# Performance work log

Hardware: AMD Instinct MI355X
Metric: run time of the kernel (lower is better)

The kernel has to match this reference:

```python
import jax, jax.numpy as jnp
import numpy as np

L_OUT, B, N, C, M, D, T = 4, 4, 1000, 80, 64, 256, 28
CLS_W, L1_W, GIOU_W, MASK_W = 2.0, 5.0, 2.0, 5.0
ALPHA, GAMMA, EPS = 0.25, 2.0, 1e-8
CANDIDATE_K, CENTER_RADIUS, BIG = 10, 2.5, 100000.0


def _areas(b):
    return (b[..., 2] - b[..., 0]) * (b[..., 3] - b[..., 1])


def pairwise_giou(b1, b2):
    # b1 [n,4], b2 [m,4] -> [n,m] generalized IoU (torchvision convention)
    area1, area2 = _areas(b1), _areas(b2)
    lt = jnp.maximum(b1[:, None, :2], b2[None, :, :2])
    rb = jnp.minimum(b1[:, None, 2:], b2[None, :, 2:])
    wh = jnp.clip(rb - lt, 0.0)
    inter = wh[..., 0] * wh[..., 1]
    union = area1[:, None] + area2[None, :] - inter
    iou = inter / union
    lti = jnp.minimum(b1[:, None, :2], b2[None, :, :2])
    rbi = jnp.maximum(b1[:, None, 2:], b2[None, :, 2:])
    whi = jnp.clip(rbi - lti, 0.0)
    areai = whi[..., 0] * whi[..., 1]
    return iou - (areai - union) / areai


def diag_giou(b1, b2):
    # elementwise giou for matched pairs, b1/b2 [n,4] -> [n]
    area1, area2 = _areas(b1), _areas(b2)
    lt = jnp.maximum(b1[:, :2], b2[:, :2])
    rb = jnp.minimum(b1[:, 2:], b2[:, 2:])
    wh = jnp.clip(rb - lt, 0.0)
    inter = wh[:, 0] * wh[:, 1]
    union = area1 + area2 - inter
    iou = inter / union
    lti = jnp.minimum(b1[:, :2], b2[:, :2])
    rbi = jnp.maximum(b1[:, 2:], b2[:, 2:])
    whi = jnp.clip(rbi - lti, 0.0)
    areai = whi[:, 0] * whi[:, 1]
    return iou - (areai - union) / areai


def pairwise_iou(b1, b2, eps=1e-8):
    # mmdet bbox_overlaps, mode='iou'
    area1, area2 = _areas(b1), _areas(b2)
    lt = jnp.maximum(b1[:, None, :2], b2[None, :, :2])
    rb = jnp.minimum(b1[:, None, 2:], b2[None, :, 2:])
    wh = jnp.clip(rb - lt, 0.0)
    inter = wh[..., 0] * wh[..., 1]
    union = jnp.maximum(area1[:, None] + area2[None, :] - inter, eps)
    return inter / union


def simota_match(logits, boxes, gt_cls, gt_boxes, img_size):
    # SimOTA assignment for one image; fixed shapes via masking instead of boolean indexing
    n, c = logits.shape
    m = gt_boxes.shape[0]
    cx = (boxes[:, 0] + boxes[:, 2]) * 0.5
    cy = (boxes[:, 1] + boxes[:, 3]) * 0.5
    w = boxes[:, 2] - boxes[:, 0]
    h = boxes[:, 3] - boxes[:, 1]
    in_gt = ((cx[:, None] > gt_boxes[None, :, 0]) & (cy[:, None] > gt_boxes[None, :, 1])
             & (cx[:, None] < gt_boxes[None, :, 2]) & (cy[:, None] < gt_boxes[None, :, 3]))
    gcx = (gt_boxes[:, 0] + gt_boxes[:, 2]) * 0.5
    gcy = (gt_boxes[:, 1] + gt_boxes[:, 3]) * 0.5
    rx = CENTER_RADIUS * w[:, None]
    ry = CENTER_RADIUS * h[:, None]
    in_ct = ((cx[:, None] > gcx[None, :] - rx) & (cx[:, None] < gcx[None, :] + rx)
             & (cy[:, None] > gcy[None, :] - ry) & (cy[:, None] < gcy[None, :] + ry))
    valid = in_gt.any(1) | in_ct.any(1)
    in_both = in_gt & in_ct
    has_valid = valid.any()
    valid = valid | (~has_valid)          # fallback: all valid when none
    in_both = in_both | (~has_valid)
    # FocalLossCost (mmdet), weight = cls weight
    p = jax.nn.sigmoid(logits)
    neg = -jnp.log(1.0 - p + EPS) * (1.0 - ALPHA) * p ** GAMMA
    pos = -jnp.log(p + EPS) * ALPHA * (1.0 - p) ** GAMMA
    cls_cost = CLS_W * (pos - neg)[:, gt_cls]          # [n,m]
    nb = boxes / img_size
    ngb = gt_boxes / img_size
    l1_cost = L1_W * jnp.abs(nb[:, None, :] - ngb[None, :, :]).sum(-1)
    giou_cost = GIOU_W * (1.0 - pairwise_giou(nb, ngb))
    cost = cls_cost + l1_cost + giou_cost + (~in_both) * BIG
    cost = jnp.where(valid[:, None], cost, 1e15)       # invalid priors never selected
    ious = pairwise_iou(boxes, gt_boxes) * valid[:, None]
    # dynamic_k_matching
    topk_ious, _ = jax.lax.top_k(ious.T, CANDIDATE_K)  # [m,10]
    dyn_k = jnp.maximum(topk_ious.sum(-1).astype(jnp.int32), 1)
    rank = jnp.argsort(jnp.argsort(cost, axis=0), axis=0)
    matching = rank < dyn_k[None, :]                   # [n,m]
    multi = matching.sum(1) > 1
    best = jnp.argmin(cost, axis=1)
    best_oh = best[:, None] == jnp.arange(m)[None, :]
    matching = jnp.where(multi[:, None], best_oh, matching)
    fg = matching.any(1)
    gt_ind = jnp.argmax(matching, axis=1)
    return fg, gt_ind


def per_image_loss(logits, boxes, pfeat, gt_cls, gt_boxes, gt_masks, img_size, w_mask):
    sg = jax.lax.stop_gradient
    fg, gt_ind = simota_match(sg(logits), sg(boxes), gt_cls, sg(gt_boxes), sg(img_size))
    c = logits.shape[1]
    gcls = gt_cls[gt_ind]
    label = jnp.where(fg[:, None], jax.nn.one_hot(gcls, c, dtype=logits.dtype), 0.0)
    # sigmoid focal loss (sum over all n*c logits)
    p = jax.nn.sigmoid(logits)
    ce = -(label * jax.nn.log_sigmoid(logits) + (1.0 - label) * jax.nn.log_sigmoid(-logits))
    p_t = p * label + (1.0 - p) * (1.0 - label)
    alpha_t = ALPHA * label + (1.0 - ALPHA) * (1.0 - label)
    cls_loss = (alpha_t * ce * (1.0 - p_t) ** GAMMA).sum()
    fgf = fg.astype(logits.dtype)
    nb = boxes / img_size
    gb = gt_boxes[gt_ind] / img_size
    l1_loss = (jnp.abs(nb - gb).sum(-1) * fgf).sum()
    giou_loss = ((1.0 - diag_giou(nb, gb)) * fgf).sum()
    # mask head: per-class mask logits from proposal feats; gather only assigned class
    d = pfeat.shape[1]
    tt = T * T
    w_sel = w_mask.reshape(d, c, tt)[:, gcls, :]        # [d,n,tt]
    m_sel = jax.nn.sigmoid(jnp.einsum('nd,dnt->nt', pfeat, w_sel))
    gm = gt_masks.reshape(gt_masks.shape[0], -1)[gt_ind]  # [n,tt]
    inter = (m_sel * gm).sum(-1)
    union = m_sel.sum(-1) + gm.sum(-1) + 1e-8
    mask_loss = ((1.0 - 2.0 * inter / union) * fgf).sum()
    return cls_loss, l1_loss, giou_loss, mask_loss, fgf.sum()


def _forward(pred_logits, pred_boxes, proposal_feat, gt_boxes, gt_masks, image_size, w_mask, gt_classes):
    per = jax.vmap(per_image_loss, in_axes=(0, 0, 0, 0, 0, 0, 0, None))
    total = jnp.zeros(4, dtype=pred_logits.dtype)
    n_out = pred_logits.shape[0]
    for l in range(n_out):   # small fixed loop over output heads
        cl, l1, gl, ml, k = per(pred_logits[l], pred_boxes[l], proposal_feat[l],
                                gt_classes, gt_boxes, gt_masks, image_size, w_mask)
        num_ins = k.sum()
        total = total + jnp.stack([cl.sum(), l1.sum(), gl.sum(), ml.sum()]) / num_ins
    weights = jnp.array([CLS_W, L1_W, GIOU_W, MASK_W], dtype=total.dtype)
    return weights * total / n_out   # [cls, l1, giou, mask] losses


def setup_inputs():
    key = jax.random.key(0)
    ks = jax.random.split(key, 8)

    def rand_boxes(k, shape):
        k1, k2 = jax.random.split(k)
        ctr = jax.random.uniform(k1, shape + (2,), minval=100.0, maxval=700.0)
        wh = jax.random.uniform(k2, shape + (2,), minval=20.0, maxval=300.0)
        return jnp.concatenate([ctr - wh * 0.5, ctr + wh * 0.5], axis=-1)

    pred_logits = jax.random.normal(ks[0], (L_OUT, B, N, C), dtype=jnp.float32)
    pred_boxes = rand_boxes(ks[1], (L_OUT, B, N))
    proposal_feat = 0.1 * jax.random.normal(ks[2], (L_OUT, B, N, D), dtype=jnp.float32)
    gt_boxes = rand_boxes(ks[3], (B, M))
    gt_masks = (jax.random.uniform(ks[4], (B, M, T, T)) > 0.5).astype(jnp.float32)
    image_size = 800.0 * jnp.ones((B,), dtype=jnp.float32)
    w_mask = 0.02 * jax.random.normal(ks[5], (D, C * T * T), dtype=jnp.float32)
    gt_classes = jax.random.randint(ks[6], (B, M), 0, C)
    return {"pred_logits": pred_logits, "pred_boxes": pred_boxes, "proposal_feat": proposal_feat,
            "gt_boxes": gt_boxes, "gt_masks": gt_masks, "image_size": image_size,
            "w_mask": w_mask, "gt_classes": gt_classes}


def reference(pred_logits, pred_boxes, proposal_feat, gt_boxes, gt_masks, image_size, w_mask, gt_classes):
    return _forward(pred_logits, pred_boxes, proposal_feat, gt_boxes, gt_masks, image_size, w_mask, gt_classes)
```

## Files before the change

### kernel.cpp

```cpp
#include <hip/hip_runtime.h>
#include <math.h>
#include <float.h>

#define LOUT 4
#define BATCH 4
#define NP 1000
#define NC 80
#define NM 64
#define ND 256
#define TT 784
#define NIMG (LOUT*BATCH)
#define CWTT (NC*TT)
#define MAXF (NIMG*NP)
#define CH 16
#define TPT 112
#define MAXCH 768

__device__ __forceinline__ float block_reduce_sum(float v, float* red) {
    int tid = threadIdx.x;
    red[tid] = v; __syncthreads();
    for (int s = blockDim.x >> 1; s > 0; s >>= 1) {
        if (tid < s) red[tid] += red[tid + s];
        __syncthreads();
    }
    float r = red[0]; __syncthreads();
    return r;
}

__global__ void __launch_bounds__(256) k_prep(
        const float* __restrict__ logits, const float* __restrict__ boxes,
        const float* __restrict__ gtb, const float* __restrict__ gtm,
        int* __restrict__ valid, unsigned long long* __restrict__ inboth,
        float* __restrict__ logT, float* __restrict__ negsum,
        float* __restrict__ gmsum, float* __restrict__ interA,
        float* __restrict__ msumA, float* __restrict__ accum, int* __restrict__ cnt) {
    int blk = blockIdx.x;
    int tid = threadIdx.x;
    __shared__ float red[256];
    __shared__ float tile[32][33];
    if (blk < 256) {
        int bj = blk;
        float s = 0.f;
        for (int t = tid; t < TT; t += 256) s += gtm[(size_t)bj * TT + t];
        float r = block_reduce_sum(s, red);
        if (tid == 0) gmsum[bj] = r;
    } else if (blk < 320) {
        int rel = blk - 256;
        int img = rel >> 2, q = rel & 3, b = img % BATCH;
        float* g = red;
        g[tid] = gtb[b * NM * 4 + tid];
        __syncthreads();
        int i = q * 256 + tid;
        if (i >= NP) return;
        float4 bx = *(const float4*)&boxes[((size_t)img * NP + i) * 4];
        float x0 = bx.x, y0 = bx.y, x1 = bx.z, y1 = bx.w;
        float cx = (x0 + x1) * 0.5f, cy = (y0 + y1) * 0.5f;
        float w = x1 - x0, h = y1 - y0;
        float rx = 2.5f * w, ry = 2.5f * h;
        bool any_gt = false, any_ct = false;
        unsigned long long ib = 0ull;
        for (int j = 0; j < NM; ++j) {
            float gx0 = g[j*4], gy0 = g[j*4+1], gx1 = g[j*4+2], gy1 = g[j*4+3];
            bool igt = (cx > gx0) && (cy > gy0) && (cx < gx1) && (cy < gy1);
            float gcx = (gx0 + gx1) * 0.5f, gcy = (gy0 + gy1) * 0.5f;
            bool ict = (cx > gcx - rx) && (cx < gcx + rx) && (cy > gcy - ry) && (cy < gcy + ry);
            any_gt |= igt; any_ct |= ict;
            if (igt && ict) ib |= (1ull << j);
        }
        bool v = any_gt || any_ct;
        valid[img * NP + i] = v ? 1 : 0;
        inboth[img * NP + i] = ib;
    } else if (blk < 1856) {
        int rel = blk - 320;
        int img = rel / 96; int r2 = rel % 96;
        int i0 = (r2 / 3) * 32, c0 = (r2 % 3) * 32;
        int tx = tid & 31, ty4 = tid >> 5;
        #pragma unroll
        for (int r = 0; r < 4; ++r) {
            int ty = ty4 + r * 8;
            int i = i0 + ty, c = c0 + tx;
            tile[ty][tx] = (i < NP && c < NC) ? logits[((size_t)img * NP + i) * NC + c] : 0.f;
        }
        __syncthreads();
        #pragma unroll
        for (int r = 0; r < 4; ++r) {
            int ty = ty4 + r * 8;
            int c = c0 + ty, i = i0 + tx;
            if (c < NC && i < NP) logT[((size_t)img * NC + c) * NP + i] = tile[tx][ty];
        }
    } else if (blk < 1920) {
        int rel = blk - 1856;
        int img = rel >> 2, q = rel & 3;
        int i = q * 256 + tid;
        if (i >= NP) return;
        const float* lr = logits + ((size_t)img * NP + i) * NC;
        float s = 0.f;
        #pragma unroll 4
        for (int c = 0; c < NC; ++c) {
            float x = lr[c];
            float p = 1.f / (1.f + expf(-x));
            float ax = fabsf(x);
            float sp = log1pf(expf(-ax));
            float ls_neg = fminf(-x, 0.f) - sp;
            s += 0.75f * (-ls_neg) * p * p;
        }
        negsum[img * NP + i] = s;
    } else if (blk < 2045) {
        int idx = (blk - 1920) * 256 + tid;
        if (idx < 16000) interA[idx] = 0.f;
        else if (idx < 32000) msumA[idx - 16000] = 0.f;
    } else {
        if (tid < 80) accum[tid] = 0.f;
        else if (tid < 160) cnt[tid - 80] = 0;
    }
}

__global__ void __launch_bounds__(256) k_costtopk(
        const float* __restrict__ logT, const float* __restrict__ boxes,
        const float* __restrict__ gtb, const int* __restrict__ gcls_all,
        const float* __restrict__ imsz,
        const int* __restrict__ valid, const unsigned long long* __restrict__ inboth,
        float* __restrict__ cost, float* __restrict__ kthc, int* __restrict__ kthi) {
    int img = blockIdx.y, b = img % BATCH;
    int tid = threadIdx.x;
    int w = tid >> 6, l = tid & 63;
    int j = blockIdx.x * 4 + w;
    float s = imsz[b], inv_s = 1.f / s;
    const float* gj = gtb + (b * NM + j) * 4;
    float gx0 = gj[0], gy0 = gj[1], gx1 = gj[2], gy1 = gj[3];
    int gc = gcls_all[b * NM + j];
    float garea = (gx1 - gx0) * (gy1 - gy0);
    float ngx0 = gx0 * inv_s, ngy0 = gy0 * inv_s, ngx1 = gx1 * inv_s, ngy1 = gy1 * inv_s;
    float ngarea = (ngx1 - ngx0) * (ngy1 - ngy0);
    size_t colbase = ((size_t)img * NM + j) * NP;
    const float* lrow = logT + ((size_t)img * NC + gc) * NP;
    unsigned vmask = 0, ibmask = 0;
    #pragma unroll
    for (int e = 0; e < 16; ++e) {
        int i = e * 64 + l;
        if (i < NP) {
            if (valid[img * NP + i]) vmask |= 1u << e;
            if ((inboth[img * NP + i] >> j) & 1ull) ibmask |= 1u << e;
        }
    }
    int hv = __any(vmask != 0);
    float icv[16], ccv[16];
    #pragma unroll
    for (int e = 0; e < 16; ++e) {
        int i = e * 64 + l;
        if (i < NP) {
            float4 bx = *(const float4*)&boxes[((size_t)img * NP + i) * 4];
            float x0 = bx.x, y0 = bx.y, x1 = bx.z, y1 = bx.w;
            float area = (x1 - x0) * (y1 - y0);
            float ltx = fmaxf(x0, gx0), lty = fmaxf(y0, gy0);
            float rbx = fminf(x1, gx1), rby = fminf(y1, gy1);
            float iw = fmaxf(rbx - ltx, 0.f), ih = fmaxf(rby - lty, 0.f);
            float inter = iw * ih;
            float uni = fmaxf(area + garea - inter, 1e-8f);
            float iou = inter / uni;
            float nx0 = x0 * inv_s, ny0 = y0 * inv_s, nx1 = x1 * inv_s, ny1 = y1 * inv_s;
            float narea = (nx1 - nx0) * (ny1 - ny0);
            float nltx = fmaxf(nx0, ngx0), nlty = fmaxf(ny0, ngy0);
            float nrbx = fminf(nx1, ngx1), nrby = fminf(ny1, ngy1);
            float niw = fmaxf(nrbx - nltx, 0.f), nih = fmaxf(nrby - nlty, 0.f);
            float ninter = niw * nih;
            float nuni = narea + ngarea - ninter;
            float niou = ninter / nuni;
            float ex0 = fminf(nx0, ngx0), ey0 = fminf(ny0, ngy0);
            float ex1 = fmaxf(nx1, ngx1), ey1 = fmaxf(ny1, ngy1);
            float earea = fmaxf(ex1 - ex0, 0.f) * fmaxf(ey1 - ey0, 0.f);
            float giou = niou - (earea - nuni) / earea;
            float giou_cost = 2.f * (1.f - giou);
            float l1 = 5.f * (fabsf(nx0 - ngx0) + fabsf(ny0 - ngy0) + fabsf(nx1 - ngx1) + fabsf(ny1 - ngy1));
            float x = lrow[i];
            float p = 1.f / (1.f + expf(-x));
            float neg = -logf(1.f - p + 1e-8f) * 0.75f * p * p;
            float pos = -logf(p + 1e-8f) * 0.25f * (1.f - p) * (1.f - p);
            float cls = 2.f * (pos - neg);
            bool vld = ((vmask >> e) & 1u) || (hv == 0);
            bool inb = ((ibmask >> e) & 1u) || (hv == 0);
            float cst = cls + l1 + giou_cost + (inb ? 0.f : 100000.f);
            if (!vld) cst = 1e15f;
            cost[colbase + i] = cst;
            ccv[e] = cst;
            icv[e] = vld ? iou : 0.f;
        } else {
            ccv[e] = FLT_MAX;
            icv[e] = -FLT_MAX;
        }
    }
    unsigned cons = 0;
    float ssum = 0.f;
    for (int it = 0; it < 10; ++it) {
        float bv = -FLT_MAX; int bi = 0x7fffffff;
        #pragma unroll
        for (int e = 0; e < 16; ++e) {
            if (cons & (1u << e)) continue;
            float v = icv[e]; int i = e * 64 + l;
            if ((v > bv) || (v == bv && i < bi)) { bv = v; bi = i; }
        }
        #pragma unroll
        for (int sft = 1; sft < 64; sft <<= 1) {
            float ov = __shfl_xor(bv, sft, 64);
            int oi = __shfl_xor(bi, sft, 64);
            if ((ov > bv) || (ov == bv && oi < bi)) { bv = ov; bi = oi; }
        }
        ssum += bv;
        if ((bi & 63) == l) cons |= 1u << (bi >> 6);
    }
    int dk = (int)ssum; if (dk < 1) dk = 1;
    cons = 0;
    float gv = 0.f; int gi = 0;
    for (int it = 0; it < dk; ++it) {
        float bv = FLT_MAX; int bi = 0x7fffffff;
        #pragma unroll
        for (int e = 0; e < 16; ++e) {
            if (cons & (1u << e)) continue;
            float v = ccv[e]; int i = e * 64 + l;
            if ((v < bv) || (v == bv && i < bi)) { bv = v; bi = i; }
        }
        #pragma unroll
        for (int sft = 1; sft < 64; sft <<= 1) {
            float ov = __shfl_xor(bv, sft, 64);
            int oi = __shfl_xor(bi, sft, 64);
            if ((ov < bv) || (ov == bv && oi < bi)) { bv = ov; bi = oi; }
        }
        if ((bi & 63) == l) cons |= 1u << (bi >> 6);
        gv = bv; gi = bi;
    }
    if (l == 0) { kthc[img * NM + j] = gv; kthi[img * NM + j] = gi; }
}

__global__ void k_match(const float* __restrict__ cost,
                        const float* __restrict__ kthc, const int* __restrict__ kthi,
                        const float* __restrict__ boxes, const float* __restrict__ gtb,
                        const float* __restrict__ imsz, const int* __restrict__ gcls_all,
                        const float* __restrict__ negsum, const float* __restrict__ logT,
                        int* __restrict__ fg, int* __restrict__ gt_ind,
                        int* __restrict__ cnt, float* __restrict__ accum) {
    int img = blockIdx.y, b = img % BATCH;
    int i = blockIdx.x * blockDim.x + threadIdx.x;
    __shared__ float skc[NM]; __shared__ int ski[NM];
    __shared__ float red[256];
    if (threadIdx.x < NM) {
        skc[threadIdx.x] = kthc[img * NM + threadIdx.x];
        ski[threadIdx.x] = kthi[img * NM + threadIdx.x];
    }
    __syncthreads();
    float l1 = 0.f, gl = 0.f, f = 0.f, vcls = 0.f;
    if (i < NP) {
        vcls = negsum[img * NP + i];
        int cntm = 0, first = -1;
        float bc = FLT_MAX; int bj = 0;
        for (int j = 0; j < NM; ++j) {
            float c = cost[((size_t)img * NM + j) * NP + i];
            bool m = (c < skc[j]) || (c == skc[j] && i <= ski[j]);
            if (m) { cntm++; if (first < 0) first = j; }
            if (c < bc) { bc = c; bj = j; }
        }
        int gi = 0, isfg = 0;
        if (cntm > 1) { gi = bj; isfg = 1; }
        else if (cntm == 1) { gi = first; isfg = 1; }
        fg[img * NP + i] = isfg;
        gt_ind[img * NP + i] = gi;
        if (isfg) {
            int gc = gcls_all[b * NM + gi];
            atomicAdd(&cnt[gc], 1);
            float x = logT[((size_t)img * NC + gc) * NP + i];
            float p = 1.f / (1.f + expf(-x));
            float ax = fabsf(x);
            float sp = log1pf(expf(-ax));
            float ls_pos = fminf(x, 0.f) - sp;
            float ls_neg = fminf(-x, 0.f) - sp;
            float pos = 0.25f * (-ls_pos) * (1.f - p) * (1.f - p);
            float neg = 0.75f * (-ls_neg) * p * p;
            vcls += pos - neg;
            float inv = 1.f / imsz[b];
            float4 bx = *(const float4*)&boxes[((size_t)img * NP + i) * 4];
            const float* gj = gtb + (b * NM + gi) * 4;
            float nx0 = bx.x*inv, ny0 = bx.y*inv, nx1 = bx.z*inv, ny1 = bx.w*inv;
            float gx0 = gj[0]*inv, gy0 = gj[1]*inv, gx1 = gj[2]*inv, gy1 = gj[3]*inv;
            l1 = fabsf(nx0-gx0) + fabsf(ny0-gy0) + fabsf(nx1-gx1) + fabsf(ny1-gy1);
            float a1 = (nx1-nx0)*(ny1-ny0), a2 = (gx1-gx0)*(gy1-gy0);
            float ltx = fmaxf(nx0,gx0), lty = fmaxf(ny0,gy0);
            float rbx = fminf(nx1,gx1), rby = fminf(ny1,gy1);
            float iw = fmaxf(rbx-ltx,0.f), ih = fmaxf(rby-lty,0.f);
            float inter = iw*ih, uni = a1+a2-inter, iou = inter/uni;
            float ex0 = fminf(nx0,gx0), ey0 = fminf(ny0,gy0);
            float ex1 = fmaxf(nx1,gx1), ey1 = fmaxf(ny1,gy1);
            float ea = fmaxf(ex1-ex0,0.f)*fmaxf(ey1-ey0,0.f);
            float giou = iou - (ea-uni)/ea;
            gl = 1.f - giou;
            f = 1.f;
        }
    }
    float scl = block_reduce_sum(vcls, red);
    float sl1 = block_reduce_sum(l1, red);
    float sgl = block_reduce_sum(gl, red);
    float sf  = block_reduce_sum(f, red);
    if (threadIdx.x == 0) {
        atomicAdd(&accum[img*5+0], scl);
        atomicAdd(&accum[img*5+1], sl1);
        atomicAdd(&accum[img*5+2], sgl);
        atomicAdd(&accum[img*5+4], sf);
    }
}

__global__ void __launch_bounds__(1024) k_scanscatter(
        const int* __restrict__ cnt, const int* __restrict__ fg,
        const int* __restrict__ gti, const int* __restrict__ gcls,
        int* __restrict__ offs_g, int* __restrict__ total,
        int* __restrict__ chtab, int* __restrict__ nch, int* __restrict__ list) {
    __shared__ int offs[NC]; __shared__ int choff[NC]; __shared__ int sfill[NC];
    int tid = threadIdx.x;
    if (tid == 0) {
        int s = 0, m = 0;
        for (int c = 0; c < NC; ++c) {
            offs[c] = s; s += cnt[c];
            choff[c] = m; m += (cnt[c] + CH - 1) / CH;
        }
        *total = s; *nch = m;
    }
    if (tid < NC) sfill[tid] = 0;
    __syncthreads();
    if (tid < NC) {
        offs_g[tid] = offs[tid];
        int n = cnt[tid], co = choff[tid];
        for (int k = 0; k * CH < n; ++k) chtab[co + k] = (tid << 16) | k;
    }
    for (int idx = tid; idx < NIMG * NP; idx += 1024) {
        if (fg[idx]) {
            int img = idx / NP, i = idx % NP, b = img % BATCH;
            int gt = gti[idx];
            int c = gcls[b * NM + gt];
            int pos = offs[c] + atomicAdd(&sfill[c], 1);
            list[pos] = (img << 16) | (gt << 10) | i;
        }
    }
}

__global__ void __launch_bounds__(128) k_mgemm(
        const float* __restrict__ pfeat, const float* __restrict__ wmask,
        const float* __restrict__ gtm, const int* __restrict__ list,
        const int* __restrict__ cnt, const int* __restrict__ offs,
        const int* __restrict__ chtab, const int* __restrict__ nch,
        float* __restrict__ inter, float* __restrict__ msum) {
    int ch = blockIdx.x;
    if (ch >= *nch) return;
    int e = chtab[ch];
    int c = e >> 16, k = e & 0xffff;
    int base = offs[c] + k * CH;
    int P = min(CH, cnt[c] - k * CH);
    int tid = threadIdx.x;
    bool act = (tid < TPT);
    int t = blockIdx.y * TPT + (act ? tid : 0);
    __shared__ float pf[CH][ND];
    __shared__ int sl[CH];
    if (tid < CH) sl[tid] = (tid < P) ? list[base + tid] : 0;
    __syncthreads();
    for (int idx = tid; idx < CH * (ND / 4); idx += 128) {
        int p = idx >> 6, d4 = idx & 63;
        float4 v = {0.f, 0.f, 0.f, 0.f};
        if (p < P) {
            int pk = sl[p];
            int img = pk >> 16, i = pk & 1023;
            v = *(const float4*)&pfeat[((size_t)img * NP + i) * ND + d4 * 4];
        }
        *(float4*)&pf[p][d4 * 4] = v;
    }
    __syncthreads();
    float acc[CH];
    #pragma unroll
    for (int p = 0; p < CH; ++p) acc[p] = 0.f;
    if (act) {
        const float* wr = wmask + (size_t)c * TT + t;
        float4 wq[4];
        #pragma unroll
        for (int q = 0; q < 4; ++q) {
            const float* wp = wr + (size_t)q * 4 * CWTT;
            wq[q].x = wp[0]; wq[q].y = wp[CWTT];
            wq[q].z = wp[2 * (size_t)CWTT]; wq[q].w = wp[3 * (size_t)CWTT];
        }
        #pragma unroll 4
        for (int d4 = 0; d4 < 60; ++d4) {
            float4 w = wq[d4 & 3];
            const float* wp = wr + (size_t)(d4 + 4) * 4 * CWTT;
            wq[d4 & 3].x = wp[0]; wq[d4 & 3].y = wp[CWTT];
            wq[d4 & 3].z = wp[2 * (size_t)CWTT]; wq[d4 & 3].w = wp[3 * (size_t)CWTT];
            int d = d4 * 4;
            #pragma unroll
            for (int p = 0; p < CH; ++p) {
                float4 q4 = *(const float4*)&pf[p][d];
                acc[p] += q4.x * w.x + q4.y * w.y + q4.z * w.z + q4.w * w.w;
            }
        }
        #pragma unroll
        for (int d4 = 60; d4 < 64; ++d4) {
            float4 w = wq[d4 & 3];
            int d = d4 * 4;
            #pragma unroll
            for (int p = 0; p < CH; ++p) {
                float4 q4 = *(const float4*)&pf[p][d];
                acc[p] += q4.x * w.x + q4.y * w.y + q4.z * w.z + q4.w * w.w;
            }
        }
    }
    #pragma unroll 4
    for (int p = 0; p < CH; ++p) {
        if (p >= P) break;
        int pk = sl[p];
        int img = pk >> 16, j = (pk >> 10) & 63, b = img % BATCH;
        float li = 0.f, lm = 0.f;
        if (act) {
            float m = 1.f / (1.f + expf(-acc[p]));
            float g = gtm[((size_t)(b * NM + j)) * TT + t];
            li = m * g; lm = m;
        }
        #pragma unroll
        for (int s = 32; s > 0; s >>= 1) {
            li += __shfl_down(li, s, 64);
            lm += __shfl_down(lm, s, 64);
        }
        if ((tid & 63) == 0) {
            atomicAdd(&inter[base + p], li);
            atomicAdd(&msum[base + p], lm);
        }
    }
}

__global__ void __launch_bounds__(256) k_dicefinal(
        const int* __restrict__ list, const int* __restrict__ total,
        const float* __restrict__ inter, const float* __restrict__ msum,
        const float* __restrict__ gmsum, const float* __restrict__ accum,
        float* __restrict__ out) {
    __shared__ float md[NIMG];
    int tid = threadIdx.x;
    if (tid < NIMG) md[tid] = 0.f;
    __syncthreads();
    int n = *total;
    for (int e = tid; e < n; e += 256) {
        int pk = list[e];
        int img = pk >> 16, j = (pk >> 10) & 63, b = img % BATCH;
        float d = 1.f - 2.f * inter[e] / (msum[e] + gmsum[b * NM + j] + 1e-8f);
        atomicAdd(&md[img], d);
    }
    __syncthreads();
    if (tid == 0) {
        float tot[4] = {0.f, 0.f, 0.f, 0.f};
        for (int l = 0; l < LOUT; ++l) {
            float s0 = 0.f, s1 = 0.f, s2 = 0.f, s3 = 0.f, s4 = 0.f;
            for (int b = 0; b < BATCH; ++b) {
                int img = l * BATCH + b;
                s0 += accum[img*5+0]; s1 += accum[img*5+1]; s2 += accum[img*5+2];
                s3 += md[img];        s4 += accum[img*5+4];
            }
            tot[0] += s0 / s4; tot[1] += s1 / s4; tot[2] += s2 / s4; tot[3] += s3 / s4;
        }
        const float w[4] = {2.f, 5.f, 2.f, 5.f};
        for (int k = 0; k < 4; ++k) out[k] = w[k] * tot[k] / (float)LOUT;
    }
}

extern "C" void kernel_launch(void* const* d_in, const int* in_sizes, int n_in,
                              void* d_out, int out_size, void* d_ws, size_t ws_size,
                              hipStream_t stream) {
    const float* logits = (const float*)d_in[0];
    const float* boxes  = (const float*)d_in[1];
    const float* pfeat  = (const float*)d_in[2];
    const float* gtb    = (const float*)d_in[3];
    const float* gtm    = (const float*)d_in[4];
    const float* imsz   = (const float*)d_in[5];
    const float* wmask  = (const float*)d_in[6];
    const int*   gcls   = (const int*)d_in[7];

    char* ws = (char*)d_ws;
    size_t off = 0;
    auto alloc = [&](size_t bytes) -> void* {
        void* p = ws + off;
        off = (off + bytes + 255) & ~(size_t)255;
        return p;
    };
    float* accum = (float*)alloc(NIMG * 5 * sizeof(float));
    int* cnt    = (int*)alloc(NC * sizeof(int));
    float* interA = (float*)alloc((size_t)MAXF * sizeof(float));
    float* msumA  = (float*)alloc((size_t)MAXF * sizeof(float));
    float* cost = (float*)alloc((size_t)NIMG * NM * NP * sizeof(float));
    float* logT = (float*)alloc((size_t)NIMG * NC * NP * sizeof(float));
    float* negsum = (float*)alloc((size_t)NIMG * NP * sizeof(float));
    int* valid  = (int*)alloc((size_t)NIMG * NP * sizeof(int));
    unsigned long long* inboth = (unsigned long long*)alloc((size_t)NIMG * NP * sizeof(unsigned long long));
    float* kthc = (float*)alloc(NIMG * NM * sizeof(float));
    int* kthi   = (int*)alloc(NIMG * NM * sizeof(int));
    int* fg     = (int*)alloc((size_t)NIMG * NP * sizeof(int));
    int* gti    = (int*)alloc((size_t)NIMG * NP * sizeof(int));
    float* gmsum = (float*)alloc(BATCH * NM * sizeof(float));
    int* offs   = (int*)alloc(NC * sizeof(int));
    int* total  = (int*)alloc(sizeof(int));
    int* nch    = (int*)alloc(sizeof(int));
    int* chtab  = (int*)alloc((size_t)MAXCH * sizeof(int));
    int* list   = (int*)alloc((size_t)MAXF * sizeof(int));

    k_prep<<<2046, 256, 0, stream>>>(logits, boxes, gtb, gtm, valid, inboth,
                                     logT, negsum, gmsum, interA, msumA, accum, cnt);
    k_costtopk<<<dim3(NM / 4, NIMG), 256, 0, stream>>>(logT, boxes, gtb, gcls, imsz, valid, inboth, cost, kthc, kthi);
    k_match<<<dim3((NP + 255) / 256, NIMG), 256, 0, stream>>>(cost, kthc, kthi, boxes, gtb, imsz, gcls, negsum, logT, fg, gti, cnt, accum);
    k_scanscatter<<<1, 1024, 0, stream>>>(cnt, fg, gti, gcls, offs, total, chtab, nch, list);
    k_mgemm<<<dim3(MAXCH, 7), 128, 0, stream>>>(pfeat, wmask, gtm, list, cnt, offs, chtab, nch, interA, msumA);
    k_dicefinal<<<1, 256, 0, stream>>>(list, total, interA, msumA, gmsum, accum, (float*)d_out);
}
```

Baseline: 193.1 us.

## Fuse front stages into cooperative persistent kernel and fold dice final into mgemm

Merges the prep, cost/top-k, match and scan/scatter kernels into one cooperative kernel that uses grid-wide syncs between phases. It also folds the final dice reduction into the mask GEMM kernel through a last-block-done atomic counter. The aim is to cut kernel launch and inter-kernel gaps across six small dependent stages. In exchange it adds grid.sync costs and limits the grid to co-resident blocks, which can reduce parallelism in the phases that have few blocks.

```diff
diff --git a/kernel.cpp b/kernel.cpp
--- a/kernel.cpp
+++ b/kernel.cpp
@@ -1,6 +1,9 @@
 #include <hip/hip_runtime.h>
+#include <hip/hip_cooperative_groups.h>
 #include <math.h>
 #include <float.h>
+
+namespace cg = cooperative_groups;
 
 #define LOUT 4
 #define BATCH 4
@@ -15,6 +18,7 @@
 #define CH 16
 #define TPT 112
 #define MAXCH 768
+#define TOTALB (MAXCH*7)
 
 __device__ __forceinline__ float block_reduce_sum(float v, float* red) {
     int tid = threadIdx.x;
@@ -27,313 +31,309 @@
     return r;
 }
 
-__global__ void __launch_bounds__(256) k_prep(
+__global__ void __launch_bounds__(256) k_front(
         const float* __restrict__ logits, const float* __restrict__ boxes,
         const float* __restrict__ gtb, const float* __restrict__ gtm,
+        const int* __restrict__ gcls, const float* __restrict__ imsz,
         int* __restrict__ valid, unsigned long long* __restrict__ inboth,
         float* __restrict__ logT, float* __restrict__ negsum,
-        float* __restrict__ gmsum, float* __restrict__ interA,
-        float* __restrict__ msumA, float* __restrict__ accum, int* __restrict__ cnt) {
-    int blk = blockIdx.x;
+        float* __restrict__ gmsum, float* __restrict__ interA, float* __restrict__ msumA,
+        float* __restrict__ accum, int* __restrict__ cnt, int* __restrict__ fill,
+        float* __restrict__ cost, float* __restrict__ kthc, int* __restrict__ kthi,
+        int* __restrict__ fg, int* __restrict__ gti,
+        int* __restrict__ offs_g, int* __restrict__ total, int* __restrict__ chtab,
+        int* __restrict__ nch, int* __restrict__ list, int* __restrict__ done, int G) {
+    cg::grid_group grid = cg::this_grid();
     int tid = threadIdx.x;
     __shared__ float red[256];
     __shared__ float tile[32][33];
-    if (blk < 256) {
-        int bj = blk;
-        float s = 0.f;
-        for (int t = tid; t < TT; t += 256) s += gtm[(size_t)bj * TT + t];
-        float r = block_reduce_sum(s, red);
-        if (tid == 0) gmsum[bj] = r;
-    } else if (blk < 320) {
-        int rel = blk - 256;
-        int img = rel >> 2, q = rel & 3, b = img % BATCH;
-        float* g = red;
-        g[tid] = gtb[b * NM * 4 + tid];
-        __syncthreads();
-        int i = q * 256 + tid;
-        if (i >= NP) return;
-        float4 bx = *(const float4*)&boxes[((size_t)img * NP + i) * 4];
-        float x0 = bx.x, y0 = bx.y, x1 = bx.z, y1 = bx.w;
-        float cx = (x0 + x1) * 0.5f, cy = (y0 + y1) * 0.5f;
-        float w = x1 - x0, h = y1 - y0;
-        float rx = 2.5f * w, ry = 2.5f * h;
-        bool any_gt = false, any_ct = false;
-        unsigned long long ib = 0ull;
-        for (int j = 0; j < NM; ++j) {
-            float gx0 = g[j*4], gy0 = g[j*4+1], gx1 = g[j*4+2], gy1 = g[j*4+3];
-            bool igt = (cx > gx0) && (cy > gy0) && (cx < gx1) && (cy < gy1);
-            float gcx = (gx0 + gx1) * 0.5f, gcy = (gy0 + gy1) * 0.5f;
-            bool ict = (cx > gcx - rx) && (cx < gcx + rx) && (cy > gcy - ry) && (cy < gcy + ry);
-            any_gt |= igt; any_ct |= ict;
-            if (igt && ict) ib |= (1ull << j);
-        }
-        bool v = any_gt || any_ct;
-        valid[img * NP + i] = v ? 1 : 0;
-        inboth[img * NP + i] = ib;
-    } else if (blk < 1856) {
-        int rel = blk - 320;
-        int img = rel / 96; int r2 = rel % 96;
-        int i0 = (r2 / 3) * 32, c0 = (r2 % 3) * 32;
-        int tx = tid & 31, ty4 = tid >> 5;
-        #pragma unroll
-        for (int r = 0; r < 4; ++r) {
-            int ty = ty4 + r * 8;
-            int i = i0 + ty, c = c0 + tx;
-            tile[ty][tx] = (i < NP && c < NC) ? logits[((size_t)img * NP + i) * NC + c] : 0.f;
-        }
-        __syncthreads();
-        #pragma unroll
-        for (int r = 0; r < 4; ++r) {
-            int ty = ty4 + r * 8;
-            int c = c0 + ty, i = i0 + tx;
-            if (c < NC && i < NP) logT[((size_t)img * NC + c) * NP + i] = tile[tx][ty];
-        }
-    } else if (blk < 1920) {
-        int rel = blk - 1856;
-        int img = rel >> 2, q = rel & 3;
-        int i = q * 256 + tid;
-        if (i >= NP) return;
-        const float* lr = logits + ((size_t)img * NP + i) * NC;
-        float s = 0.f;
-        #pragma unroll 4
-        for (int c = 0; c < NC; ++c) {
-            float x = lr[c];
-            float p = 1.f / (1.f + expf(-x));
-            float ax = fabsf(x);
-            float sp = log1pf(expf(-ax));
-            float ls_neg = fminf(-x, 0.f) - sp;
-            s += 0.75f * (-ls_neg) * p * p;
-        }
-        negsum[img * NP + i] = s;
-    } else if (blk < 2045) {
-        int idx = (blk - 1920) * 256 + tid;
-        if (idx < 16000) interA[idx] = 0.f;
-        else if (idx < 32000) msumA[idx - 16000] = 0.f;
-    } else {
-        if (tid < 80) accum[tid] = 0.f;
-        else if (tid < 160) cnt[tid - 80] = 0;
-    }
-}
-
-__global__ void __launch_bounds__(256) k_costtopk(
-        const float* __restrict__ logT, const float* __restrict__ boxes,
-        const float* __restrict__ gtb, const int* __restrict__ gcls_all,
-        const float* __restrict__ imsz,
-        const int* __restrict__ valid, const unsigned long long* __restrict__ inboth,
-        float* __restrict__ cost, float* __restrict__ kthc, int* __restrict__ kthi) {
-    int img = blockIdx.y, b = img % BATCH;
-    int tid = threadIdx.x;
-    int w = tid >> 6, l = tid & 63;
-    int j = blockIdx.x * 4 + w;
-    float s = imsz[b], inv_s = 1.f / s;
-    const float* gj = gtb + (b * NM + j) * 4;
-    float gx0 = gj[0], gy0 = gj[1], gx1 = gj[2], gy1 = gj[3];
-    int gc = gcls_all[b * NM + j];
-    float garea = (gx1 - gx0) * (gy1 - gy0);
-    float ngx0 = gx0 * inv_s, ngy0 = gy0 * inv_s, ngx1 = gx1 * inv_s, ngy1 = gy1 * inv_s;
-    float ngarea = (ngx1 - ngx0) * (ngy1 - ngy0);
-    size_t colbase = ((size_t)img * NM + j) * NP;
-    const float* lrow = logT + ((size_t)img * NC + gc) * NP;
-    unsigned vmask = 0, ibmask = 0;
-    #pragma unroll
-    for (int e = 0; e < 16; ++e) {
-        int i = e * 64 + l;
-        if (i < NP) {
-            if (valid[img * NP + i]) vmask |= 1u << e;
-            if ((inboth[img * NP + i] >> j) & 1ull) ibmask |= 1u << e;
-        }
-    }
-    int hv = __any(vmask != 0);
-    float icv[16], ccv[16];
-    #pragma unroll
-    for (int e = 0; e < 16; ++e) {
-        int i = e * 64 + l;
-        if (i < NP) {
-            float4 bx = *(const float4*)&boxes[((size_t)img * NP + i) * 4];
-            float x0 = bx.x, y0 = bx.y, x1 = bx.z, y1 = bx.w;
-            float area = (x1 - x0) * (y1 - y0);
-            float ltx = fmaxf(x0, gx0), lty = fmaxf(y0, gy0);
-            float rbx = fminf(x1, gx1), rby = fminf(y1, gy1);
-            float iw = fmaxf(rbx - ltx, 0.f), ih = fmaxf(rby - lty, 0.f);
-            float inter = iw * ih;
-            float uni = fmaxf(area + garea - inter, 1e-8f);
-            float iou = inter / uni;
-            float nx0 = x0 * inv_s, ny0 = y0 * inv_s, nx1 = x1 * inv_s, ny1 = y1 * inv_s;
-            float narea = (nx1 - nx0) * (ny1 - ny0);
-            float nltx = fmaxf(nx0, ngx0), nlty = fmaxf(ny0, ngy0);
-            float nrbx = fminf(nx1, ngx1), nrby = fminf(ny1, ngy1);
-            float niw = fmaxf(nrbx - nltx, 0.f), nih = fmaxf(nrby - nlty, 0.f);
-            float ninter = niw * nih;
-            float nuni = narea + ngarea - ninter;
-            float niou = ninter / nuni;
-            float ex0 = fminf(nx0, ngx0), ey0 = fminf(ny0, ngy0);
-            float ex1 = fmaxf(nx1, ngx1), ey1 = fmaxf(ny1, ngy1);
-            float earea = fmaxf(ex1 - ex0, 0.f) * fmaxf(ey1 - ey0, 0.f);
-            float giou = niou - (earea - nuni) / earea;
-            float giou_cost = 2.f * (1.f - giou);
-            float l1 = 5.f * (fabsf(nx0 - ngx0) + fabsf(ny0 - ngy0) + fabsf(nx1 - ngx1) + fabsf(ny1 - ngy1));
-            float x = lrow[i];
-            float p = 1.f / (1.f + expf(-x));
-            float neg = -logf(1.f - p + 1e-8f) * 0.75f * p * p;
-            float pos = -logf(p + 1e-8f) * 0.25f * (1.f - p) * (1.f - p);
-            float cls = 2.f * (pos - neg);
-            bool vld = ((vmask >> e) & 1u) || (hv == 0);
-            bool inb = ((ibmask >> e) & 1u) || (hv == 0);
-            float cst = cls + l1 + giou_cost + (inb ? 0.f : 100000.f);
-            if (!vld) cst = 1e15f;
-            cost[colbase + i] = cst;
-            ccv[e] = cst;
-            icv[e] = vld ? iou : 0.f;
+    __shared__ float skc[NM]; __shared__ int ski[NM];
+    __shared__ int loffs[NC]; __shared__ int lchoff[NC];
+
+    for (int vb = blockIdx.x; vb < 2046; vb += G) {
+        if (vb < 256) {
+            int bj = vb;
+            float s = 0.f;
+            for (int t = tid; t < TT; t += 256) s += gtm[(size_t)bj * TT + t];
+            float r = block_reduce_sum(s, red);
+            if (tid == 0) gmsum[bj] = r;
+        } else if (vb < 320) {
+            int rel = vb - 256;
+            int img = rel >> 2, q = rel & 3, b = img % BATCH;
+            red[tid] = gtb[b * NM * 4 + tid];
+            __syncthreads();
+            int i = q * 256 + tid;
+            if (i < NP) {
+                float4 bx = *(const float4*)&boxes[((size_t)img * NP + i) * 4];
+                float x0 = bx.x, y0 = bx.y, x1 = bx.z, y1 = bx.w;
+                float cx = (x0 + x1) * 0.5f, cy = (y0 + y1) * 0.5f;
+                float w = x1 - x0, h = y1 - y0;
+                float rx = 2.5f * w, ry = 2.5f * h;
+                bool any_gt = false, any_ct = false;
+                unsigned long long ib = 0ull;
+                for (int j = 0; j < NM; ++j) {
+                    float gx0 = red[j*4], gy0 = red[j*4+1], gx1 = red[j*4+2], gy1 = red[j*4+3];
+                    bool igt = (cx > gx0) && (cy > gy0) && (cx < gx1) && (cy < gy1);
+                    float gcx = (gx0 + gx1) * 0.5f, gcy = (gy0 + gy1) * 0.5f;
+                    bool ict = (cx > gcx - rx) && (cx < gcx + rx) && (cy > gcy - ry) && (cy < gcy + ry);
+                    any_gt |= igt; any_ct |= ict;
+                    if (igt && ict) ib |= (1ull << j);
+                }
+                valid[img * NP + i] = (any_gt || any_ct) ? 1 : 0;
+                inboth[img * NP + i] = ib;
+            }
+        } else if (vb < 1856) {
+            int rel = vb - 320;
+            int img = rel / 96; int r2 = rel % 96;
+            int i0 = (r2 / 3) * 32, c0 = (r2 % 3) * 32;
+            int tx = tid & 31, ty4 = tid >> 5;
+            #pragma unroll
+            for (int r = 0; r < 4; ++r) {
+                int ty = ty4 + r * 8;
+                int i = i0 + ty, c = c0 + tx;
+                tile[ty][tx] = (i < NP && c < NC) ? logits[((size_t)img * NP + i) * NC + c] : 0.f;
+            }
+            __syncthreads();
+            #pragma unroll
+            for (int r = 0; r < 4; ++r) {
+                int ty = ty4 + r * 8;
+                int c = c0 + ty, i = i0 + tx;
+                if (c < NC && i < NP) logT[((size_t)img * NC + c) * NP + i] = tile[tx][ty];
+            }
+        } else if (vb < 1920) {
+            int rel = vb - 1856;
+            int img = rel >> 2, q = rel & 3;
+            int i = q * 256 + tid;
+            if (i < NP) {
+                const float* lr = logits + ((size_t)img * NP + i) * NC;
+                float s = 0.f;
+                #pragma unroll 4
+                for (int c = 0; c < NC; ++c) {
+                    float x = lr[c];
+                    float p = 1.f / (1.f + expf(-x));
+                    float ax = fabsf(x);
+                    float sp = log1pf(expf(-ax));
+                    float ls_neg = fminf(-x, 0.f) - sp;
+                    s += 0.75f * (-ls_neg) * p * p;
+                }
+                negsum[img * NP + i] = s;
+            }
+        } else if (vb < 2045) {
+            int idx = (vb - 1920) * 256 + tid;
+            if (idx < 16000) interA[idx] = 0.f;
+            else if (idx < 32000) msumA[idx - 16000] = 0.f;
         } else {
-            ccv[e] = FLT_MAX;
-            icv[e] = -FLT_MAX;
-        }
-    }
-    unsigned cons = 0;
-    float ssum = 0.f;
-    for (int it = 0; it < 10; ++it) {
-        float bv = -FLT_MAX; int bi = 0x7fffffff;
+            if (tid < 80) accum[tid] = 0.f;
+            else if (tid < 160) cnt[tid - 80] = 0;
+            else if (tid < 240) fill[tid - 160] = 0;
+            else if (tid == 240) *done = 0;
+        }
+        __syncthreads();
+    }
+    grid.sync();
+
+    for (int vb = blockIdx.x; vb < 256; vb += G) {
+        int img = vb >> 4, b = img % BATCH;
+        int w = tid >> 6, l = tid & 63;
+        int j = ((vb & 15) << 2) + w;
+        float s = imsz[b], inv_s = 1.f / s;
+        const float* gj = gtb + (b * NM + j) * 4;
+        float gx0 = gj[0], gy0 = gj[1], gx1 = gj[2], gy1 = gj[3];
+        int gc = gcls[b * NM + j];
+        float garea = (gx1 - gx0) * (gy1 - gy0);
+        float ngx0 = gx0 * inv_s, ngy0 = gy0 * inv_s, ngx1 = gx1 * inv_s, ngy1 = gy1 * inv_s;
+        float ngarea = (ngx1 - ngx0) * (ngy1 - ngy0);
+        size_t colbase = ((size_t)img * NM + j) * NP;
+        const float* lrow = logT + ((size_t)img * NC + gc) * NP;
+        unsigned vmask = 0, ibmask = 0;
         #pragma unroll
         for (int e = 0; e < 16; ++e) {
-            if (cons & (1u << e)) continue;
-            float v = icv[e]; int i = e * 64 + l;
-            if ((v > bv) || (v == bv && i < bi)) { bv = v; bi = i; }
-        }
-        #pragma unroll
-        for (int sft = 1; sft < 64; sft <<= 1) {
-            float ov = __shfl_xor(bv, sft, 64);
-            int oi = __shfl_xor(bi, sft, 64);
-            if ((ov > bv) || (ov == bv && oi < bi)) { bv = ov; bi = oi; }
-        }
-        ssum += bv;
-        if ((bi & 63) == l) cons |= 1u << (bi >> 6);
-    }
-    int dk = (int)ssum; if (dk < 1) dk = 1;
-    cons = 0;
-    float gv = 0.f; int gi = 0;
-    for (int it = 0; it < dk; ++it) {
-        float bv = FLT_MAX; int bi = 0x7fffffff;
+            int i = e * 64 + l;
+            if (i < NP) {
+                if (valid[img * NP + i]) vmask |= 1u << e;
+                if ((inboth[img * NP + i] >> j) & 1ull) ibmask |= 1u << e;
+            }
+        }
+        int hv = __any(vmask != 0);
+        float icv[16], ccv[16];
         #pragma unroll
         for (int e = 0; e < 16; ++e) {
-            if (cons & (1u << e)) continue;
-            float v = ccv[e]; int i = e * 64 + l;
-            if ((v < bv) || (v == bv && i < bi)) { bv = v; bi = i; }
-        }
-        #pragma unroll
-        for (int sft = 1; sft < 64; sft <<= 1) {
-            float ov = __shfl_xor(bv, sft, 64);
-            int oi = __shfl_xor(bi, sft, 64);
-            if ((ov < bv) || (ov == bv && oi < bi)) { bv = ov; bi = oi; }
-        }
-        if ((bi & 63) == l) cons |= 1u << (bi >> 6);
-        gv = bv; gi = bi;
-    }
-    if (l == 0) { kthc[img * NM + j] = gv; kthi[img * NM + j] = gi; }
-}
-
-__global__ void k_match(const float* __restrict__ cost,
-                        const float* __restrict__ kthc, const int* __restrict__ kthi,
-                        const float* __restrict__ boxes, const float* __restrict__ gtb,
-                        const float* __restrict__ imsz, const int* __restrict__ gcls_all,
-                        const float* __restrict__ negsum, const float* __restrict__ logT,
-                        int* __restrict__ fg, int* __restrict__ gt_ind,
-                        int* __restrict__ cnt, float* __restrict__ accum) {
-    int img = blockIdx.y, b = img % BATCH;
-    int i = blockIdx.x * blockDim.x + threadIdx.x;
-    __shared__ float skc[NM]; __shared__ int ski[NM];
-    __shared__ float red[256];
-    if (threadIdx.x < NM) {
-        skc[threadIdx.x] = kthc[img * NM + threadIdx.x];
-        ski[threadIdx.x] = kthi[img * NM + threadIdx.x];
-    }
-    __syncthreads();
-    float l1 = 0.f, gl = 0.f, f = 0.f, vcls = 0.f;
-    if (i < NP) {
-        vcls = negsum[img * NP + i];
-        int cntm = 0, first = -1;
-        float bc = FLT_MAX; int bj = 0;
-        for (int j = 0; j < NM; ++j) {
-            float c = cost[((size_t)img * NM + j) * NP + i];
-            bool m = (c < skc[j]) || (c == skc[j] && i <= ski[j]);
-            if (m) { cntm++; if (first < 0) first = j; }
-            if (c < bc) { bc = c; bj = j; }
-        }
-        int gi = 0, isfg = 0;
-        if (cntm > 1) { gi = bj; isfg = 1; }
-        else if (cntm == 1) { gi = first; isfg = 1; }
-        fg[img * NP + i] = isfg;
-        gt_ind[img * NP + i] = gi;
-        if (isfg) {
-            int gc = gcls_all[b * NM + gi];
-            atomicAdd(&cnt[gc], 1);
-            float x = logT[((size_t)img * NC + gc) * NP + i];
-            float p = 1.f / (1.f + expf(-x));
-            float ax = fabsf(x);
-            float sp = log1pf(expf(-ax));
-            float ls_pos = fminf(x, 0.f) - sp;
-            float ls_neg = fminf(-x, 0.f) - sp;
-            float pos = 0.25f * (-ls_pos) * (1.f - p) * (1.f - p);
-            float neg = 0.75f * (-ls_neg) * p * p;
-            vcls += pos - neg;
-            float inv = 1.f / imsz[b];
-            float4 bx = *(const float4*)&boxes[((size_t)img * NP + i) * 4];
-            const float* gj = gtb + (b * NM + gi) * 4;
-            float nx0 = bx.x*inv, ny0 = bx.y*inv, nx1 = bx.z*inv, ny1 = bx.w*inv;
-            float gx0 = gj[0]*inv, gy0 = gj[1]*inv, gx1 = gj[2]*inv, gy1 = gj[3]*inv;
-            l1 = fabsf(nx0-gx0) + fabsf(ny0-gy0) + fabsf(nx1-gx1) + fabsf(ny1-gy1);
-            float a1 = (nx1-nx0)*(ny1-ny0), a2 = (gx1-gx0)*(gy1-gy0);
-            float ltx = fmaxf(nx0,gx0), lty = fmaxf(ny0,gy0);
-            float rbx = fminf(nx1,gx1), rby = fminf(ny1,gy1);
-            float iw = fmaxf(rbx-ltx,0.f), ih = fmaxf(rby-lty,0.f);
-            float inter = iw*ih, uni = a1+a2-inter, iou = inter/uni;
-            float ex0 = fminf(nx0,gx0), ey0 = fminf(ny0,gy0);
-            float ex1 = fmaxf(nx1,gx1), ey1 = fmaxf(ny1,gy1);
-            float ea = fmaxf(ex1-ex0,0.f)*fmaxf(ey1-ey0,0.f);
-            float giou = iou - (ea-uni)/ea;
-            gl = 1.f - giou;
-            f = 1.f;
-        }
-    }
-    float scl = block_reduce_sum(vcls, red);
-    float sl1 = block_reduce_sum(l1, red);
-    float sgl = block_reduce_sum(gl, red);
-    float sf  = block_reduce_sum(f, red);
-    if (threadIdx.x == 0) {
-        atomicAdd(&accum[img*5+0], scl);
-        atomicAdd(&accum[img*5+1], sl1);
-        atomicAdd(&accum[img*5+2], sgl);
-        atomicAdd(&accum[img*5+4], sf);
-    }
-}
-
-__global__ void __launch_bounds__(1024) k_scanscatter(
-        const int* __restrict__ cnt, const int* __restrict__ fg,
-        const int* __restrict__ gti, const int* __restrict__ gcls,
-        int* __restrict__ offs_g, int* __restrict__ total,
-        int* __restrict__ chtab, int* __restrict__ nch, int* __restrict__ list) {
-    __shared__ int offs[NC]; __shared__ int choff[NC]; __shared__ int sfill[NC];
-    int tid = threadIdx.x;
+            int i = e * 64 + l;
+            if (i < NP) {
+                float4 bx = *(const float4*)&boxes[((size_t)img * NP + i) * 4];
+                float x0 = bx.x, y0 = bx.y, x1 = bx.z, y1 = bx.w;
+                float area = (x1 - x0) * (y1 - y0);
+                float ltx = fmaxf(x0, gx0), lty = fmaxf(y0, gy0);
+                float rbx = fminf(x1, gx1), rby = fminf(y1, gy1);
+                float iw = fmaxf(rbx - ltx, 0.f), ih = fmaxf(rby - lty, 0.f);
+                float inter = iw * ih;
+                float uni = fmaxf(area + garea - inter, 1e-8f);
+                float iou = inter / uni;
+                float nx0 = x0 * inv_s, ny0 = y0 * inv_s, nx1 = x1 * inv_s, ny1 = y1 * inv_s;
+                float narea = (nx1 - nx0) * (ny1 - ny0);
+                float nltx = fmaxf(nx0, ngx0), nlty = fmaxf(ny0, ngy0);
+                float nrbx = fminf(nx1, ngx1), nrby = fminf(ny1, ngy1);
+                float niw = fmaxf(nrbx - nltx, 0.f), nih = fmaxf(nrby - nlty, 0.f);
+                float ninter = niw * nih;
+                float nuni = narea + ngarea - ninter;
+                float niou = ninter / nuni;
+                float ex0 = fminf(nx0, ngx0), ey0 = fminf(ny0, ngy0);
+                float ex1 = fmaxf(nx1, ngx1), ey1 = fmaxf(ny1, ngy1);
+                float earea = fmaxf(ex1 - ex0, 0.f) * fmaxf(ey1 - ey0, 0.f);
+                float giou = niou - (earea - nuni) / earea;
+                float giou_cost = 2.f * (1.f - giou);
+                float l1 = 5.f * (fabsf(nx0 - ngx0) + fabsf(ny0 - ngy0) + fabsf(nx1 - ngx1) + fabsf(ny1 - ngy1));
+                float x = lrow[i];
+                float p = 1.f / (1.f + expf(-x));
+                float neg = -logf(1.f - p + 1e-8f) * 0.75f * p * p;
+                float pos = -logf(p + 1e-8f) * 0.25f * (1.f - p) * (1.f - p);
+                float cls = 2.f * (pos - neg);
+                bool vld = ((vmask >> e) & 1u) || (hv == 0);
+                bool inb = ((ibmask >> e) & 1u) || (hv == 0);
+                float cst = cls + l1 + giou_cost + (inb ? 0.f : 100000.f);
+                if (!vld) cst = 1e15f;
+                cost[colbase + i] = cst;
+                ccv[e] = cst;
+                icv[e] = vld ? iou : 0.f;
+            } else {
+                ccv[e] = FLT_MAX;
+                icv[e] = -FLT_MAX;
+            }
+        }
+        unsigned cons = 0;
+        float ssum = 0.f;
+        for (int it = 0; it < 10; ++it) {
+            float bv = -FLT_MAX; int bi = 0x7fffffff;
+            #pragma unroll
+            for (int e = 0; e < 16; ++e) {
+                if (cons & (1u << e)) continue;
+                float v = icv[e]; int i = e * 64 + l;
+                if ((v > bv) || (v == bv && i < bi)) { bv = v; bi = i; }
+            }
+            #pragma unroll
+            for (int sft = 1; sft < 64; sft <<= 1) {
+                float ov = __shfl_xor(bv, sft, 64);
+                int oi = __shfl_xor(bi, sft, 64);
+                if ((ov > bv) || (ov == bv && oi < bi)) { bv = ov; bi = oi; }
+            }
+            ssum += bv;
+            if ((bi & 63) == l) cons |= 1u << (bi >> 6);
+        }
+        int dk = (int)ssum; if (dk < 1) dk = 1;
+        cons = 0;
+        float gv = 0.f; int gi = 0;
+        for (int it = 0; it < dk; ++it) {
+            float bv = FLT_MAX; int bi = 0x7fffffff;
+            #pragma unroll
+            for (int e = 0; e < 16; ++e) {
+                if (cons & (1u << e)) continue;
+                float v = ccv[e]; int i = e * 64 + l;
+                if ((v < bv) || (v == bv && i < bi)) { bv = v; bi = i; }
+            }
+            #pragma unroll
+            for (int sft = 1; sft < 64; sft <<= 1) {
+                float ov = __shfl_xor(bv, sft, 64);
+                int oi = __shfl_xor(bi, sft, 64);
+                if ((ov < bv) || (ov == bv && oi < bi)) { bv = ov; bi = oi; }
+            }
+            if ((bi & 63) == l) cons |= 1u << (bi >> 6);
+            gv = bv; gi = bi;
+        }
+        if (l == 0) { kthc[img * NM + j] = gv; kthi[img * NM + j] = gi; }
+    }
+    grid.sync();
+
+    for (int vb = blockIdx.x; vb < 64; vb += G) {
+        int img = vb >> 2, b = img % BATCH;
+        int i = ((vb & 3) << 8) + tid;
+        if (tid < NM) {
+            skc[tid] = kthc[img * NM + tid];
+            ski[tid] = kthi[img * NM + tid];
+        }
+        __syncthreads();
+        float l1 = 0.f, gl = 0.f, f = 0.f, vcls = 0.f;
+        if (i < NP) {
+            vcls = negsum[img * NP + i];
+            int cntm = 0, first = -1;
+            float bc = FLT_MAX; int bj = 0;
+            for (int j = 0; j < NM; ++j) {
+                float c = cost[((size_t)img * NM + j) * NP + i];
+                bool m = (c < skc[j]) || (c == skc[j] && i <= ski[j]);
+                if (m) { cntm++; if (first < 0) first = j; }
+                if (c < bc) { bc = c; bj = j; }
+            }
+            int gi = 0, isfg = 0;
+            if (cntm > 1) { gi = bj; isfg = 1; }
+            else if (cntm == 1) { gi = first; isfg = 1; }
+            fg[img * NP + i] = isfg;
+            gti[img * NP + i] = gi;
+            if (isfg) {
+                int gc = gcls[b * NM + gi];
+                atomicAdd(&cnt[gc], 1);
+                float x = logT[((size_t)img * NC + gc) * NP + i];
+                float p = 1.f / (1.f + expf(-x));
+                float ax = fabsf(x);
+                float sp = log1pf(expf(-ax));
+                float ls_pos = fminf(x, 0.f) - sp;
+                float ls_neg = fminf(-x, 0.f) - sp;
+                float pos = 0.25f * (-ls_pos) * (1.f - p) * (1.f - p);
+                float neg = 0.75f * (-ls_neg) * p * p;
+                vcls += pos - neg;
+                float inv = 1.f / imsz[b];
+                float4 bx = *(const float4*)&boxes[((size_t)img * NP + i) * 4];
+                const float* gj = gtb + (b * NM + gi) * 4;
+                float nx0 = bx.x*inv, ny0 = bx.y*inv, nx1 = bx.z*inv, ny1 = bx.w*inv;
+                float gx0 = gj[0]*inv, gy0 = gj[1]*inv, gx1 = gj[2]*inv, gy1 = gj[3]*inv;
+                l1 = fabsf(nx0-gx0) + fabsf(ny0-gy0) + fabsf(nx1-gx1) + fabsf(ny1-gy1);
+                float a1 = (nx1-nx0)*(ny1-ny0), a2 = (gx1-gx0)*(gy1-gy0);
+                float ltx = fmaxf(nx0,gx0), lty = fmaxf(ny0,gy0);
+                float rbx = fminf(nx1,gx1), rby = fminf(ny1,gy1);
+                float iw = fmaxf(rbx-ltx,0.f), ih = fmaxf(rby-lty,0.f);
+                float inter = iw*ih, uni = a1+a2-inter, iou = inter/uni;
+                float ex0 = fminf(nx0,gx0), ey0 = fminf(ny0,gy0);
+                float ex1 = fmaxf(nx1,gx1), ey1 = fmaxf(ny1,gy1);
+                float ea = fmaxf(ex1-ex0,0.f)*fmaxf(ey1-ey0,0.f);
+                float giou = iou - (ea-uni)/ea;
+                gl = 1.f - giou;
+                f = 1.f;
+            }
+        }
+        float scl = block_reduce_sum(vcls, red);
+        float sl1 = block_reduce_sum(l1, red);
+        float sgl = block_reduce_sum(gl, red);
+        float sf  = block_reduce_sum(f, red);
+        if (tid == 0) {
+            atomicAdd(&accum[img*5+0], scl);
+            atomicAdd(&accum[img*5+1], sl1);
+            atomicAdd(&accum[img*5+2], sgl);
+            atomicAdd(&accum[img*5+4], sf);
+        }
+        __syncthreads();
+    }
+    grid.sync();
+
     if (tid == 0) {
         int s = 0, m = 0;
         for (int c = 0; c < NC; ++c) {
-            offs[c] = s; s += cnt[c];
-            choff[c] = m; m += (cnt[c] + CH - 1) / CH;
-        }
-        *total = s; *nch = m;
-    }
-    if (tid < NC) sfill[tid] = 0;
+            loffs[c] = s; s += cnt[c];
+            lchoff[c] = m; m += (cnt[c] + CH - 1) / CH;
+        }
+        if (blockIdx.x == 0) { *total = s; *nch = m; }
+    }
     __syncthreads();
-    if (tid < NC) {
-        offs_g[tid] = offs[tid];
-        int n = cnt[tid], co = choff[tid];
-        for (int k = 0; k * CH < n; ++k) chtab[co + k] = (tid << 16) | k;
-    }
-    for (int idx = tid; idx < NIMG * NP; idx += 1024) {
+    if (blockIdx.x == 0) {
+        if (tid < NC) {
+            offs_g[tid] = loffs[tid];
+            int n = cnt[tid], co = lchoff[tid];
+            for (int k = 0; k * CH < n; ++k) chtab[co + k] = (tid << 16) | k;
+        }
+    }
+    for (int idx = blockIdx.x * 256 + tid; idx < NIMG * NP; idx += G * 256) {
         if (fg[idx]) {
             int img = idx / NP, i = idx % NP, b = img % BATCH;
             int gt = gti[idx];
             int c = gcls[b * NM + gt];
-            int pos = offs[c] + atomicAdd(&sfill[c], 1);
+            int pos = loffs[c] + atomicAdd(&fill[c], 1);
             list[pos] = (img << 16) | (gt << 10) | i;
         }
     }
@@ -344,120 +344,127 @@
         const float* __restrict__ gtm, const int* __restrict__ list,
         const int* __restrict__ cnt, const int* __restrict__ offs,
         const int* __restrict__ chtab, const int* __restrict__ nch,
-        float* __restrict__ inter, float* __restrict__ msum) {
+        float* __restrict__ inter, float* __restrict__ msum,
+        const float* __restrict__ gmsum, const int* __restrict__ total,
+        const float* __restrict__ accum, int* __restrict__ done,
+        float* __restrict__ out) {
     int ch = blockIdx.x;
-    if (ch >= *nch) return;
-    int e = chtab[ch];
-    int c = e >> 16, k = e & 0xffff;
-    int base = offs[c] + k * CH;
-    int P = min(CH, cnt[c] - k * CH);
     int tid = threadIdx.x;
-    bool act = (tid < TPT);
-    int t = blockIdx.y * TPT + (act ? tid : 0);
     __shared__ float pf[CH][ND];
     __shared__ int sl[CH];
-    if (tid < CH) sl[tid] = (tid < P) ? list[base + tid] : 0;
+    __shared__ int lastf;
+    __shared__ float md[NIMG];
+    bool active = (ch < *nch);
+    if (active) {
+        int e = chtab[ch];
+        int c = e >> 16, k = e & 0xffff;
+        int base = offs[c] + k * CH;
+        int P = min(CH, cnt[c] - k * CH);
+        bool act = (tid < TPT);
+        int t = blockIdx.y * TPT + (act ? tid : 0);
+        if (tid < CH) sl[tid] = (tid < P) ? list[base + tid] : 0;
+        __syncthreads();
+        for (int idx = tid; idx < CH * (ND / 4); idx += 128) {
+            int p = idx >> 6, d4 = idx & 63;
+            float4 v = {0.f, 0.f, 0.f, 0.f};
+            if (p < P) {
+                int pk = sl[p];
+                int img = pk >> 16, i = pk & 1023;
+                v = *(const float4*)&pfeat[((size_t)img * NP + i) * ND + d4 * 4];
+            }
+            *(float4*)&pf[p][d4 * 4] = v;
+        }
+        __syncthreads();
+        float acc[CH];
+        #pragma unroll
+        for (int p = 0; p < CH; ++p) acc[p] = 0.f;
+        if (act) {
+            const float* wr = wmask + (size_t)c * TT + t;
+            float4 wq[4];
+            #pragma unroll
+            for (int q = 0; q < 4; ++q) {
+                const float* wp = wr + (size_t)q * 4 * CWTT;
+                wq[q].x = wp[0]; wq[q].y = wp[CWTT];
+                wq[q].z = wp[2 * (size_t)CWTT]; wq[q].w = wp[3 * (size_t)CWTT];
+            }
+            #pragma unroll 4
+            for (int d4 = 0; d4 < 60; ++d4) {
+                float4 w = wq[d4 & 3];
+                const float* wp = wr + (size_t)(d4 + 4) * 4 * CWTT;
+                wq[d4 & 3].x = wp[0]; wq[d4 & 3].y = wp[CWTT];
+                wq[d4 & 3].z = wp[2 * (size_t)CWTT]; wq[d4 & 3].w = wp[3 * (size_t)CWTT];
+                int d = d4 * 4;
+                #pragma unroll
+                for (int p = 0; p < CH; ++p) {
+                    float4 q4 = *(const float4*)&pf[p][d];
+                    acc[p] += q4.x * w.x + q4.y * w.y + q4.z * w.z + q4.w * w.w;
+                }
+            }
+            #pragma unroll
+            for (int d4 = 60; d4 < 64; ++d4) {
+                float4 w = wq[d4 & 3];
+                int d = d4 * 4;
+                #pragma unroll
+                for (int p = 0; p < CH; ++p) {
+                    float4 q4 = *(const float4*)&pf[p][d];
+                    acc[p] += q4.x * w.x + q4.y * w.y + q4.z * w.z + q4.w * w.w;
+                }
+            }
+        }
+        int P2 = P;
+        #pragma unroll 4
+        for (int p = 0; p < CH; ++p) {
+            if (p >= P2) break;
+            int pk = sl[p];
+            int img = pk >> 16, j = (pk >> 10) & 63, b = img % BATCH;
+            float li = 0.f, lm = 0.f;
+            if (act) {
+                float m = 1.f / (1.f + expf(-acc[p]));
+                float g = gtm[((size_t)(b * NM + j)) * TT + t];
+                li = m * g; lm = m;
+            }
+            #pragma unroll
+            for (int s = 32; s > 0; s >>= 1) {
+                li += __shfl_down(li, s, 64);
+                lm += __shfl_down(lm, s, 64);
+            }
+            if ((tid & 63) == 0) {
+                atomicAdd(&inter[base + p], li);
+                atomicAdd(&msum[base + p], lm);
+            }
+        }
+    }
+    __threadfence();
+    if (tid == 0) lastf = (atomicAdd(done, 1) == TOTALB - 1);
     __syncthreads();
-    for (int idx = tid; idx < CH * (ND / 4); idx += 128) {
-        int p = idx >> 6, d4 = idx & 63;
-        float4 v = {0.f, 0.f, 0.f, 0.f};
-        if (p < P) {
-            int pk = sl[p];
-            int img = pk >> 16, i = pk & 1023;
-            v = *(const float4*)&pfeat[((size_t)img * NP + i) * ND + d4 * 4];
-        }
-        *(float4*)&pf[p][d4 * 4] = v;
-    }
-    __syncthreads();
-    float acc[CH];
-    #pragma unroll
-    for (int p = 0; p < CH; ++p) acc[p] = 0.f;
-    if (act) {
-        const float* wr = wmask + (size_t)c * TT + t;
-        float4 wq[4];
-        #pragma unroll
-        for (int q = 0; q < 4; ++q) {
-            const float* wp = wr + (size_t)q * 4 * CWTT;
-            wq[q].x = wp[0]; wq[q].y = wp[CWTT];
-            wq[q].z = wp[2 * (size_t)CWTT]; wq[q].w = wp[3 * (size_t)CWTT];
-        }
-        #pragma unroll 4
-        for (int d4 = 0; d4 < 60; ++d4) {
-            float4 w = wq[d4 & 3];
-            const float* wp = wr + (size_t)(d4 + 4) * 4 * CWTT;
-            wq[d4 & 3].x = wp[0]; wq[d4 & 3].y = wp[CWTT];
-            wq[d4 & 3].z = wp[2 * (size_t)CWTT]; wq[d4 & 3].w = wp[3 * (size_t)CWTT];
-            int d = d4 * 4;
-            #pragma unroll
-            for (int p = 0; p < CH; ++p) {
-                float4 q4 = *(const float4*)&pf[p][d];
-                acc[p] += q4.x * w.x + q4.y * w.y + q4.z * w.z + q4.w * w.w;
-            }
-        }
-        #pragma unroll
-        for (int d4 = 60; d4 < 64; ++d4) {
-            float4 w = wq[d4 & 3];
-            int d = d4 * 4;
-            #pragma unroll
-            for (int p = 0; p < CH; ++p) {
-                float4 q4 = *(const float4*)&pf[p][d];
-                acc[p] += q4.x * w.x + q4.y * w.y + q4.z * w.z + q4.w * w.w;
-            }
-        }
-    }
-    #pragma unroll 4
-    for (int p = 0; p < CH; ++p) {
-        if (p >= P) break;
-        int pk = sl[p];
-        int img = pk >> 16, j = (pk >> 10) & 63, b = img % BATCH;
-        float li = 0.f, lm = 0.f;
-        if (act) {
-            float m = 1.f / (1.f + expf(-acc[p]));
-            float g = gtm[((size_t)(b * NM + j)) * TT + t];
-            li = m * g; lm = m;
-        }
-        #pragma unroll
-        for (int s = 32; s > 0; s >>= 1) {
-            li += __shfl_down(li, s, 64);
-            lm += __shfl_down(lm, s, 64);
-        }
-        if ((tid & 63) == 0) {
-            atomicAdd(&inter[base + p], li);
-            atomicAdd(&msum[base + p], lm);
-        }
-    }
-}
-
-__global__ void __launch_bounds__(256) k_dicefinal(
-        const int* __restrict__ list, const int* __restrict__ total,
-        const float* __restrict__ inter, const float* __restrict__ msum,
-        const float* __restrict__ gmsum, const float* __restrict__ accum,
-        float* __restrict__ out) {
-    __shared__ float md[NIMG];
-    int tid = threadIdx.x;
-    if (tid < NIMG) md[tid] = 0.f;
-    __syncthreads();
-    int n = *total;
-    for (int e = tid; e < n; e += 256) {
-        int pk = list[e];
-        int img = pk >> 16, j = (pk >> 10) & 63, b = img % BATCH;
-        float d = 1.f - 2.f * inter[e] / (msum[e] + gmsum[b * NM + j] + 1e-8f);
-        atomicAdd(&md[img], d);
-    }
-    __syncthreads();
-    if (tid == 0) {
-        float tot[4] = {0.f, 0.f, 0.f, 0.f};
-        for (int l = 0; l < LOUT; ++l) {
-            float s0 = 0.f, s1 = 0.f, s2 = 0.f, s3 = 0.f, s4 = 0.f;
-            for (int b = 0; b < BATCH; ++b) {
-                int img = l * BATCH + b;
-                s0 += accum[img*5+0]; s1 += accum[img*5+1]; s2 += accum[img*5+2];
-                s3 += md[img];        s4 += accum[img*5+4];
-            }
-            tot[0] += s0 / s4; tot[1] += s1 / s4; tot[2] += s2 / s4; tot[3] += s3 / s4;
-        }
-        const float w[4] = {2.f, 5.f, 2.f, 5.f};
-        for (int k = 0; k < 4; ++k) out[k] = w[k] * tot[k] / (float)LOUT;
+    if (lastf) {
+        __threadfence();
+        if (tid < NIMG) md[tid] = 0.f;
+        __syncthreads();
+        int n = *total;
+        for (int e2 = tid; e2 < n; e2 += 128) {
+            int pk = list[e2];
+            int img = pk >> 16, j = (pk >> 10) & 63, b = img % BATCH;
+            float iv = __hip_atomic_load(&inter[e2], __ATOMIC_RELAXED, __HIP_MEMORY_SCOPE_AGENT);
+            float mv = __hip_atomic_load(&msum[e2], __ATOMIC_RELAXED, __HIP_MEMORY_SCOPE_AGENT);
+            float d = 1.f - 2.f * iv / (mv + gmsum[b * NM + j] + 1e-8f);
+            atomicAdd(&md[img], d);
+        }
+        __syncthreads();
+        if (tid == 0) {
+            float tot[4] = {0.f, 0.f, 0.f, 0.f};
+            for (int l = 0; l < LOUT; ++l) {
+                float s0 = 0.f, s1 = 0.f, s2 = 0.f, s3 = 0.f, s4 = 0.f;
+                for (int b = 0; b < BATCH; ++b) {
+                    int img = l * BATCH + b;
+                    s0 += accum[img*5+0]; s1 += accum[img*5+1]; s2 += accum[img*5+2];
+                    s3 += md[img];        s4 += accum[img*5+4];
+                }
+                tot[0] += s0 / s4; tot[1] += s1 / s4; tot[2] += s2 / s4; tot[3] += s3 / s4;
+            }
+            const float w[4] = {2.f, 5.f, 2.f, 5.f};
+            for (int k = 0; k < 4; ++k) out[k] = w[k] * tot[k] / (float)LOUT;
+        }
     }
 }
 
@@ -482,6 +489,8 @@
     };
     float* accum = (float*)alloc(NIMG * 5 * sizeof(float));
     int* cnt    = (int*)alloc(NC * sizeof(int));
+    int* fill   = (int*)alloc(NC * sizeof(int));
+    int* done   = (int*)alloc(sizeof(int));
     float* interA = (float*)alloc((size_t)MAXF * sizeof(float));
     float* msumA  = (float*)alloc((size_t)MAXF * sizeof(float));
     float* cost = (float*)alloc((size_t)NIMG * NM * NP * sizeof(float));
@@ -499,12 +508,26 @@
     int* nch    = (int*)alloc(sizeof(int));
     int* chtab  = (int*)alloc((size_t)MAXCH * sizeof(int));
     int* list   = (int*)alloc((size_t)MAXF * sizeof(int));
-
-    k_prep<<<2046, 256, 0, stream>>>(logits, boxes, gtb, gtm, valid, inboth,
-                                     logT, negsum, gmsum, interA, msumA, accum, cnt);
-    k_costtopk<<<dim3(NM / 4, NIMG), 256, 0, stream>>>(logT, boxes, gtb, gcls, imsz, valid, inboth, cost, kthc, kthi);
-    k_match<<<dim3((NP + 255) / 256, NIMG), 256, 0, stream>>>(cost, kthc, kthi, boxes, gtb, imsz, gcls, negsum, logT, fg, gti, cnt, accum);
-    k_scanscatter<<<1, 1024, 0, stream>>>(cnt, fg, gti, gcls, offs, total, chtab, nch, list);
-    k_mgemm<<<dim3(MAXCH, 7), 128, 0, stream>>>(pfeat, wmask, gtm, list, cnt, offs, chtab, nch, interA, msumA);
-    k_dicefinal<<<1, 256, 0, stream>>>(list, total, interA, msumA, gmsum, accum, (float*)d_out);
+    float* outp = (float*)d_out;
+
+    int nb = 0;
+    if (hipOccupancyMaxActiveBlocksPerMultiprocessor(&nb, k_front, 256, 0) != hipSuccess || nb < 1)
+        nb = 2;
+    int G = nb * 256;
+    if (G > 2048) G = 2048;
+
+    void* args[] = {
+        (void*)&logits, (void*)&boxes, (void*)&gtb, (void*)&gtm,
+        (void*)&gcls, (void*)&imsz,
+        (void*)&valid, (void*)&inboth, (void*)&logT, (void*)&negsum,
+        (void*)&gmsum, (void*)&interA, (void*)&msumA,
+        (void*)&accum, (void*)&cnt, (void*)&fill,
+        (void*)&cost, (void*)&kthc, (void*)&kthi,
+        (void*)&fg, (void*)&gti,
+        (void*)&offs, (void*)&total, (void*)&chtab,
+        (void*)&nch, (void*)&list, (void*)&done, (void*)&G
+    };
+    hipLaunchCooperativeKernel(k_front, dim3(G), dim3(256), args, 0, stream);
+    k_mgemm<<<dim3(MAXCH, 7), 128, 0, stream>>>(pfeat, wmask, gtm, list, cnt, offs, chtab, nch,
+                                                interA, msumA, gmsum, total, accum, done, outp);
 }
```

Result: slower. 467.0 us (+141.9%).
